# Performance work log

Hardware: AMD Instinct MI355X
Metric: run time of the kernel (lower is better)

## Reference

```python
import jax, jax.numpy as jnp
import numpy as np

D = 128            # actual_dim / embed_dim
DM = 2 * D         # d_model
HID = 2 * DM       # LSTMCell hidden size
NSYM = 200000
PAD = NSYM
B = 4096
S = 5
NB = 64
STEPS = 4
EPS = 1e-6


def setup_inputs() -> dict:
    key = jax.random.key(0)
    ks = jax.random.split(key, 24)
    def rn(k, sh, scale=0.02):
        return jax.random.normal(k, sh, dtype=jnp.float32) * scale
    emb = rn(ks[10], (NSYM + 1, D)).at[PAD].set(0.0)  # padding row zeroed
    inp = {
        'query': jax.random.randint(ks[0], (B, 2), 0, NSYM),
        'support': jax.random.randint(ks[1], (S, 2), 0, NSYM),
        'q_l_conn': jax.random.randint(ks[2], (B, NB, 2), 0, NSYM),
        'q_l_deg': jax.random.randint(ks[3], (B,), 0, NB),
        'q_r_conn': jax.random.randint(ks[4], (B, NB, 2), 0, NSYM),
        'q_r_deg': jax.random.randint(ks[5], (B,), 0, NB),
        's_l_conn': jax.random.randint(ks[6], (S, NB, 2), 0, NSYM),
        's_l_deg': jax.random.randint(ks[7], (S,), 0, NB),
        's_r_conn': jax.random.randint(ks[8], (S, NB, 2), 0, NSYM),
        's_r_deg': jax.random.randint(ks[9], (S,), 0, NB),
        'emb': emb,
        'gcn_w': rn(ks[11], (D, 2 * D)),
        'gcn_bias': jnp.zeros((D,), jnp.float32),
        'proj1_w': rn(ks[12], (2 * DM, DM)),
        'proj1_b': jnp.zeros((2 * DM,), jnp.float32),
        'proj2_w': rn(ks[13], (DM, 2 * DM)),
        'proj2_b': jnp.zeros((DM,), jnp.float32),
        'ln_g': jnp.ones((DM,), jnp.float32),
        'ln_b': jnp.zeros((DM,), jnp.float32),
        'w_ih': rn(ks[14], (4 * HID, DM)),
        'w_hh': rn(ks[15], (4 * HID, HID)),
        'b_ih': jnp.zeros((4 * HID,), jnp.float32),
        'b_hh': jnp.zeros((4 * HID,), jnp.float32),
    }
    return inp


def _neighbor_encoder(conn, deg, emb, gcn_w, gcn_bias):
    # conn: [N, NB, 2] ids (rel, ent); deg: [N]
    rel = emb[conn[:, :, 0]]                     # [N, NB, D] gather
    ent = emb[conn[:, :, 1]]                     # [N, NB, D] gather
    x = jnp.concatenate([rel, ent], axis=-1)     # [N, NB, 2D]
    out = jnp.einsum('bnd,kd->bnk', x, gcn_w) + gcn_bias  # [N, NB, D]
    denom = jnp.maximum(deg, 1).astype(out.dtype)[:, None]
    return jnp.tanh(out.sum(axis=1) / denom)     # [N, D]


def _support_encoder(x, proj1_w, proj1_b, proj2_w, proj2_b, ln_g, ln_b):
    residual = x
    h = jax.nn.relu(x @ proj1_w.T + proj1_b)
    h = h @ proj2_w.T + proj2_b
    z = h + residual
    mu = z.mean(axis=-1, keepdims=True)
    sigma = jnp.std(z, axis=-1, keepdims=True, ddof=1)
    return ln_g * (z - mu) / (sigma + EPS) + ln_b


def _query_encoder(support_vec, query, w_ih, w_hh, b_ih, b_hh):
    # support_vec: [DM] (single support prototype); query: [B, DM]
    bsz = query.shape[0]
    h_r = jnp.zeros((bsz, HID), query.dtype)
    c = jnp.zeros((bsz, HID), query.dtype)
    xW = query @ w_ih.T + b_ih  # invariant across steps
    h = query
    for _ in range(STEPS):
        gates = xW + h_r @ w_hh.T + b_hh
        i, f, g, o = jnp.split(gates, 4, axis=-1)
        c = jax.nn.sigmoid(f) * c + jax.nn.sigmoid(i) * jnp.tanh(g)
        h_cell = jax.nn.sigmoid(o) * jnp.tanh(c)
        h = query + h_cell[:, :DM]
        # attention over a single support row: softmax of one logit == 1
        r = jnp.broadcast_to(support_vec[None, :], h.shape)
        h_r = jnp.concatenate([h, r], axis=-1)
    return h


def reference(query, support, q_l_conn, q_l_deg, q_r_conn, q_r_deg,
              s_l_conn, s_l_deg, s_r_conn, s_r_deg,
              emb, gcn_w, gcn_bias, proj1_w, proj1_b, proj2_w, proj2_b,
              ln_g, ln_b, w_ih, w_hh, b_ih, b_hh):
    ql = _neighbor_encoder(q_l_conn, q_l_deg, emb, gcn_w, gcn_bias)
    qr = _neighbor_encoder(q_r_conn, q_r_deg, emb, gcn_w, gcn_bias)
    sl = _neighbor_encoder(s_l_conn, s_l_deg, emb, gcn_w, gcn_bias)
    sr = _neighbor_encoder(s_r_conn, s_r_deg, emb, gcn_w, gcn_bias)
    query_nb = jnp.concatenate([ql, qr], axis=-1)    # [B, DM]
    support_nb = jnp.concatenate([sl, sr], axis=-1)  # [S, DM]
    se = lambda x: _support_encoder(x, proj1_w, proj1_b, proj2_w, proj2_b, ln_g, ln_b)
    support_g = se(support_nb).mean(axis=0)          # [DM]
    query_g = se(query_nb)                            # [B, DM]
    query_f = _query_encoder(support_g, query_g, w_ih, w_hh, b_ih, b_hh)
    qn = query_f / jnp.maximum(jnp.linalg.norm(query_f, axis=-1, keepdims=True), 1e-12)
    sn = support_g / jnp.maximum(jnp.linalg.norm(support_g), 1e-12)
    return qn @ sn                                    # [B] matching scores
```

## Files before the change

kernel.cpp:

```cpp
#include <hip/hip_runtime.h>

#define BQ 4096
#define NS 5

typedef __attribute__((ext_vector_type(8))) short bf16x8;
typedef __attribute__((ext_vector_type(4))) float f32x4;
typedef unsigned short ushortT;

#define WS_QNB    0
#define WS_Z      1048576
#define WS_QG     2097152
#define WS_XW     3145728
#define WS_CBUF   5242880
#define WS_XS     6291456
#define WS_H1B    7348224
#define WS_ABF    7872512
#define WS_HB1    8134656
#define WS_P1B    8396800
#define WS_P2B    8462336
#define WS_WIHB   8527872
#define WS_WHHB   8658944
#define WS_GWB    8790016
#define WS_SNB    8806400
#define WS_H1G    8807680
#define WS_ZB     8810240
#define WS_SG     8811520
#define WS_SN     8811776
#define WS_SWL    8812032
#define WS_BL     8813056

__device__ __forceinline__ float wave_allreduce(float v) {
#pragma unroll
  for (int off = 32; off > 0; off >>= 1) v += __shfl_xor(v, off, 64);
  return v;
}
__device__ __forceinline__ float block_allreduce(float v, float* buf) {
  v = wave_allreduce(v);
  __syncthreads();
  if ((threadIdx.x & 63) == 0) buf[threadIdx.x >> 6] = v;
  __syncthreads();
  return buf[0] + buf[1] + buf[2] + buf[3];
}
__device__ __forceinline__ float sigm(float x) { return 1.0f / (1.0f + expf(-x)); }
__device__ __forceinline__ ushortT f2bf(float f) {
  unsigned int u = __float_as_uint(f);
  unsigned int r = (u + 0x7fffu + ((u >> 16) & 1u)) >> 16;
  return (ushortT)r;
}
__device__ __forceinline__ float bf2f(ushortT u) {
  return __uint_as_float(((unsigned int)u) << 16);
}
__device__ __forceinline__ float dot4(float4 a, float4 b) {
  return a.x * b.x + a.y * b.y + a.z * b.z + a.w * b.w;
}

__global__ __launch_bounds__(256) void k_gather(
    const int* __restrict__ qlc, const int* __restrict__ qrc,
    const int* __restrict__ slc, const int* __restrict__ src_,
    const float* __restrict__ emb, ushortT* __restrict__ XS,
    const float* __restrict__ w_ih, const float* __restrict__ w_hh,
    const float* __restrict__ p1w, const float* __restrict__ p2w,
    const float* __restrict__ gcn_w,
    const float* __restrict__ b_ih, const float* __restrict__ b_hh,
    ushortT* __restrict__ p1b16, ushortT* __restrict__ p2b16,
    ushortT* __restrict__ wihb, ushortT* __restrict__ whhb,
    ushortT* __restrict__ gwb, float* __restrict__ bL) {
  const int r = blockIdx.x;
  const int t = threadIdx.x;
  if (r >= 2 * (BQ + NS)) {
    const int gid = (r - 2 * (BQ + NS)) * 256 + t;
    const int stride = 512 * 256;
    for (int i = gid; i < 131072; i += stride) p1b16[i] = f2bf(p1w[i]);
    for (int i = gid; i < 131072; i += stride) p2b16[i] = f2bf(p2w[i]);
    for (int i = gid; i < 262144; i += stride) {
      int n = i >> 8, k = i & 255;
      int j = (n >> 2) + 512 * (n & 3);
      wihb[i] = f2bf(w_ih[j * 256 + k]);
      whhb[i] = f2bf(w_hh[j * 512 + k]);
    }
    for (int i = gid; i < 32768; i += stride) gwb[i] = f2bf(gcn_w[i]);
    for (int i = gid; i < 1024; i += stride) {
      int j = (i >> 2) + 512 * (i & 3);
      bL[i] = b_ih[j] + b_hh[j];
    }
    return;
  }
  const int b = r >> 1, side = r & 1;
  const int* cg;
  if (b < BQ) cg = (side ? qrc : qlc) + (size_t)b * 128;
  else        cg = (side ? src_ : slc) + (size_t)(b - BQ) * 128;
  __shared__ int connS[128];
  __shared__ __align__(16) float part[8][132];
  if (t < 128) connS[t] = cg[t];
  __syncthreads();
  const int s = t >> 5, l = t & 31;
  const float4* emb4 = (const float4*)emb;
  float4 acc = make_float4(0.f, 0.f, 0.f, 0.f);
#pragma unroll
  for (int kb = 0; kb < 2; kb++) {
    int im[8];
#pragma unroll
    for (int k = 0; k < 8; k++) im[k] = connS[(kb * 8 + k) * 8 + s];
    float4 v[8];
#pragma unroll
    for (int k = 0; k < 8; k++) v[k] = emb4[(size_t)im[k] * 32 + l];
#pragma unroll
    for (int k = 0; k < 8; k++) {
      acc.x += v[k].x; acc.y += v[k].y; acc.z += v[k].z; acc.w += v[k].w;
    }
  }
  *(float4*)&part[s][l * 4] = acc;
  __syncthreads();
  const int hf = t >> 7, dd = t & 127;
  float sum = part[hf][dd] + part[2 + hf][dd] + part[4 + hf][dd] + part[6 + hf][dd];
  XS[(size_t)r * 256 + t] = f2bf(sum);
}

__global__ __launch_bounds__(256) void k_gcn(
    const ushortT* __restrict__ XS, const ushortT* __restrict__ gwb,
    const float* __restrict__ gcn_bias,
    const int* __restrict__ qld, const int* __restrict__ qrd,
    const int* __restrict__ sld, const int* __restrict__ srd,
    float* __restrict__ qnb, float* __restrict__ snb, ushortT* __restrict__ xq) {
  __shared__ short As[64 * 40];
  __shared__ short Bs[128 * 40];
  __shared__ int degl[32], degr[32];
  const int t = threadIdx.x;
  const int row0 = blockIdx.x * 64;
  if (t < 32) {
    int b = (row0 >> 1) + t;
    int dl = 1, dr = 1;
    if (b < BQ) { dl = qld[b]; dr = qrd[b]; }
    else if (b < BQ + NS) { dl = sld[b - BQ]; dr = srd[b - BQ]; }
    degl[t] = (dl > 0) ? dl : 1;
    degr[t] = (dr > 0) ? dr : 1;
  }
  const int wave = t >> 6, lane = t & 63;
  const int wm = wave >> 1, wn = wave & 1, quad = lane >> 4, mr = lane & 15;
  f32x4 acc[2][4];
#pragma unroll
  for (int mi = 0; mi < 2; mi++)
#pragma unroll
    for (int ni = 0; ni < 4; ni++) acc[mi][ni] = (f32x4){0.f, 0.f, 0.f, 0.f};
  const int arow = t >> 2, akc = t & 3;
  for (int k0 = 0; k0 < 256; k0 += 32) {
    float4 av = *(const float4*)(XS + (size_t)(row0 + arow) * 256 + k0 + akc * 8);
    float4 bv0 = *(const float4*)(gwb + (size_t)arow * 256 + k0 + akc * 8);
    float4 bv1 = *(const float4*)(gwb + (size_t)(64 + arow) * 256 + k0 + akc * 8);
    __syncthreads();
    *(float4*)&As[arow * 40 + akc * 8] = av;
    *(float4*)&Bs[arow * 40 + akc * 8] = bv0;
    *(float4*)&Bs[(64 + arow) * 40 + akc * 8] = bv1;
    __syncthreads();
    bf16x8 af[2], bfr[4];
#pragma unroll
    for (int mi = 0; mi < 2; mi++)
      af[mi] = *(const bf16x8*)&As[(wm * 32 + mi * 16 + mr) * 40 + quad * 8];
#pragma unroll
    for (int ni = 0; ni < 4; ni++)
      bfr[ni] = *(const bf16x8*)&Bs[(wn * 64 + ni * 16 + mr) * 40 + quad * 8];
#pragma unroll
    for (int mi = 0; mi < 2; mi++)
#pragma unroll
      for (int ni = 0; ni < 4; ni++)
        acc[mi][ni] = __builtin_amdgcn_mfma_f32_16x16x32_bf16(af[mi], bfr[ni], acc[mi][ni], 0, 0, 0);
  }
#pragma unroll
  for (int mi = 0; mi < 2; mi++) {
#pragma unroll
    for (int ni = 0; ni < 4; ni++) {
      const int col = wn * 64 + ni * 16 + mr;
      const int rb = row0 + wm * 32 + mi * 16 + quad * 4;
      const float bs = 64.0f * gcn_bias[col];
#pragma unroll
      for (int reg = 0; reg < 4; reg++) {
        const int row = rb + reg;
        const int b = row >> 1, side = row & 1;
        if (b >= BQ + NS) continue;
        const int li = (row >> 1) - (row0 >> 1);
        const int deg = side ? degr[li] : degl[li];
        float val = tanhf((acc[mi][ni][reg] + bs) / (float)deg);
        if (b < BQ) {
          const size_t o = (size_t)b * 256 + side * 128 + col;
          qnb[o] = val;
          xq[o] = f2bf(val);
        } else {
          snb[(size_t)(b - BQ) * 256 + side * 128 + col] = val;
        }
      }
    }
  }
}

__global__ __launch_bounds__(256) void k_proj1(
    const ushortT* __restrict__ A, const ushortT* __restrict__ B,
    const float* __restrict__ bias, ushortT* __restrict__ outb,
    const float* __restrict__ snb, const float* __restrict__ p1w,
    const float* __restrict__ p1b, float* __restrict__ h1g) {
  __shared__ short As[64 * 40];
  __shared__ short Bs[128 * 40];
  const int t = threadIdx.x;
  if (blockIdx.x >= 256) {
    const int w = (blockIdx.x - 256) * 4 + (t >> 6);
    const int lane = t & 63;
    const int r = w >> 9, j = w & 511;
    float4 x = *(const float4*)&snb[r * 256 + lane * 4];
    float4 wv = *(const float4*)&p1w[(size_t)j * 256 + lane * 4];
    float s = wave_allreduce(dot4(x, wv));
    if (lane == 0) h1g[r * 512 + j] = fmaxf(s + p1b[j], 0.f);
    return;
  }
  const int bn = blockIdx.x % 4, bm = blockIdx.x / 4;
  const int row0 = bm * 64, col0 = bn * 128;
  const int wave = t >> 6, lane = t & 63;
  const int wm = wave >> 1, wn = wave & 1, quad = lane >> 4, mr = lane & 15;
  f32x4 acc[2][4];
#pragma unroll
  for (int mi = 0; mi < 2; mi++)
#pragma unroll
    for (int ni = 0; ni < 4; ni++) acc[mi][ni] = (f32x4){0.f, 0.f, 0.f, 0.f};
  const int arow = t >> 2, akc = t & 3;
  for (int k0 = 0; k0 < 256; k0 += 32) {
    float4 av = *(const float4*)(A + (size_t)(row0 + arow) * 256 + k0 + akc * 8);
    float4 bv0 = *(const float4*)(B + (size_t)(col0 + arow) * 256 + k0 + akc * 8);
    float4 bv1 = *(const float4*)(B + (size_t)(col0 + 64 + arow) * 256 + k0 + akc * 8);
    __syncthreads();
    *(float4*)&As[arow * 40 + akc * 8] = av;
    *(float4*)&Bs[arow * 40 + akc * 8] = bv0;
    *(float4*)&Bs[(64 + arow) * 40 + akc * 8] = bv1;
    __syncthreads();
    bf16x8 af[2], bfr[4];
#pragma unroll
    for (int mi = 0; mi < 2; mi++)
      af[mi] = *(const bf16x8*)&As[(wm * 32 + mi * 16 + mr) * 40 + quad * 8];
#pragma unroll
    for (int ni = 0; ni < 4; ni++)
      bfr[ni] = *(const bf16x8*)&Bs[(wn * 64 + ni * 16 + mr) * 40 + quad * 8];
#pragma unroll
    for (int mi = 0; mi < 2; mi++)
#pragma unroll
      for (int ni = 0; ni < 4; ni++)
        acc[mi][ni] = __builtin_amdgcn_mfma_f32_16x16x32_bf16(af[mi], bfr[ni], acc[mi][ni], 0, 0, 0);
  }
#pragma unroll
  for (int mi = 0; mi < 2; mi++) {
#pragma unroll
    for (int ni = 0; ni < 4; ni++) {
      const int col = col0 + wn * 64 + ni * 16 + mr;
      const int rb = row0 + wm * 32 + mi * 16 + quad * 4;
      const float bs = bias[col];
#pragma unroll
      for (int reg = 0; reg < 4; reg++) {
        const int row = rb + reg;
        outb[(size_t)row * 512 + col] = f2bf(fmaxf(acc[mi][ni][reg] + bs, 0.f));
      }
    }
  }
}

__global__ __launch_bounds__(256) void k_proj2(
    const ushortT* __restrict__ A, const ushortT* __restrict__ B,
    const float* __restrict__ bias, const float* __restrict__ aux,
    float* __restrict__ outf,
    const float* __restrict__ snb, const float* __restrict__ h1g,
    const float* __restrict__ p2w, const float* __restrict__ p2b,
    float* __restrict__ zb) {
  __shared__ short As[64 * 40];
  __shared__ short Bs[128 * 40];
  const int t = threadIdx.x;
  if (blockIdx.x >= 128) {
    const int w = (blockIdx.x - 128) * 4 + (t >> 6);
    const int lane = t & 63;
    const int r = w >> 8, tt = w & 255;
    float4 h0 = *(const float4*)&h1g[r * 512 + lane * 4];
    float4 h1 = *(const float4*)&h1g[r * 512 + 256 + lane * 4];
    float4 w0 = *(const float4*)&p2w[(size_t)tt * 512 + lane * 4];
    float4 w1 = *(const float4*)&p2w[(size_t)tt * 512 + 256 + lane * 4];
    float s = wave_allreduce(dot4(h0, w0) + dot4(h1, w1));
    if (lane == 0) zb[r * 256 + tt] = s + p2b[tt] + snb[r * 256 + tt];
    return;
  }
  const int bn = blockIdx.x % 2, bm = blockIdx.x / 2;
  const int row0 = bm * 64, col0 = bn * 128;
  const int wave = t >> 6, lane = t & 63;
  const int wm = wave >> 1, wn = wave & 1, quad = lane >> 4, mr = lane & 15;
  f32x4 acc[2][4];
#pragma unroll
  for (int mi = 0; mi < 2; mi++)
#pragma unroll
    for (int ni = 0; ni < 4; ni++) acc[mi][ni] = (f32x4){0.f, 0.f, 0.f, 0.f};
  const int arow = t >> 2, akc = t & 3;
  for (int k0 = 0; k0 < 512; k0 += 32) {
    float4 av = *(const float4*)(A + (size_t)(row0 + arow) * 512 + k0 + akc * 8);
    float4 bv0 = *(const float4*)(B + (size_t)(col0 + arow) * 512 + k0 + akc * 8);
    float4 bv1 = *(const float4*)(B + (size_t)(col0 + 64 + arow) * 512 + k0 + akc * 8);
    __syncthreads();
    *(float4*)&As[arow * 40 + akc * 8] = av;
    *(float4*)&Bs[arow * 40 + akc * 8] = bv0;
    *(float4*)&Bs[(64 + arow) * 40 + akc * 8] = bv1;
    __syncthreads();
    bf16x8 af[2], bfr[4];
#pragma unroll
    for (int mi = 0; mi < 2; mi++)
      af[mi] = *(const bf16x8*)&As[(wm * 32 + mi * 16 + mr) * 40 + quad * 8];
#pragma unroll
    for (int ni = 0; ni < 4; ni++)
      bfr[ni] = *(const bf16x8*)&Bs[(wn * 64 + ni * 16 + mr) * 40 + quad * 8];
#pragma unroll
    for (int mi = 0; mi < 2; mi++)
#pragma unroll
      for (int ni = 0; ni < 4; ni++)
        acc[mi][ni] = __builtin_amdgcn_mfma_f32_16x16x32_bf16(af[mi], bfr[ni], acc[mi][ni], 0, 0, 0);
  }
#pragma unroll
  for (int mi = 0; mi < 2; mi++) {
#pragma unroll
    for (int ni = 0; ni < 4; ni++) {
      const int col = col0 + wn * 64 + ni * 16 + mr;
      const int rb = row0 + wm * 32 + mi * 16 + quad * 4;
      const float bs = bias[col];
#pragma unroll
      for (int reg = 0; reg < 4; reg++) {
        const int row = rb + reg;
        const size_t off = (size_t)row * 256 + col;
        outf[off] = acc[mi][ni][reg] + bs + aux[off];
      }
    }
  }
}

__global__ __launch_bounds__(256) void k_ln2(
    const float* __restrict__ Z, const float* __restrict__ ln_g,
    const float* __restrict__ ln_b, float* __restrict__ qg, ushortT* __restrict__ qgb,
    const float* __restrict__ zb, float* __restrict__ sg, float* __restrict__ sn_out) {
  const int t = threadIdx.x;
  if (blockIdx.x >= BQ / 4) {
    __shared__ float rbuf[4];
    float acc = 0.f;
    for (int r = 0; r < NS; r++) {
      float z = zb[r * 256 + t];
      float s = block_allreduce(z, rbuf);
      float mu = s * (1.f / 256.f);
      float dz = z - mu;
      float s2 = block_allreduce(dz * dz, rbuf);
      float rstd = 1.f / (sqrtf(s2 * (1.f / 255.f)) + 1e-6f);
      acc += ln_g[t] * dz * rstd + ln_b[t];
      __syncthreads();
    }
    float g = acc * (1.f / (float)NS);
    sg[t] = g;
    float n2 = block_allreduce(g * g, rbuf);
    sn_out[t] = g / fmaxf(sqrtf(n2), 1e-12f);
    return;
  }
  const int row = blockIdx.x * 4 + (t >> 6);
  const int lane = t & 63;
  float4 z = *(const float4*)&Z[(size_t)row * 256 + lane * 4];
  float s = wave_allreduce(z.x + z.y + z.z + z.w);
  float mu = s * (1.f / 256.f);
  float dx = z.x - mu, dy = z.y - mu, dz = z.z - mu, dw = z.w - mu;
  float s2 = wave_allreduce(dx * dx + dy * dy + dz * dz + dw * dw);
  float rstd = 1.f / (sqrtf(s2 * (1.f / 255.f)) + 1e-6f);
  float4 g = *(const float4*)&ln_g[lane * 4];
  float4 bb = *(const float4*)&ln_b[lane * 4];
  float4 o;
  o.x = g.x * dx * rstd + bb.x;
  o.y = g.y * dy * rstd + bb.y;
  o.z = g.z * dz * rstd + bb.z;
  o.w = g.w * dw * rstd + bb.w;
  *(float4*)&qg[(size_t)row * 256 + lane * 4] = o;
  ushort4 u;
  u.x = f2bf(o.x); u.y = f2bf(o.y); u.z = f2bf(o.z); u.w = f2bf(o.w);
  *(ushort4*)&qgb[(size_t)row * 256 + lane * 4] = u;
}

__global__ __launch_bounds__(256) void k_gemm_lstm(
    const ushortT* __restrict__ A, const ushortT* __restrict__ B,
    const float* __restrict__ bL, float* __restrict__ sWl,
    const float* __restrict__ qg, ushortT* __restrict__ xwb,
    float* __restrict__ cbuf, ushortT* __restrict__ hb_out,
    const float* __restrict__ sg, const float* __restrict__ w_hh, int phase) {
  __shared__ short As[64 * 40];
  __shared__ short Bs[128 * 40];
  __shared__ __align__(16) float Cs[64 * 132];
  const int t = threadIdx.x;
  if (blockIdx.x >= 512) {
    const int n = (blockIdx.x - 512) * 4 + (t >> 6);
    const int lane = t & 63;
    const int j = (n >> 2) + 512 * (n & 3);
    float4 x = *(const float4*)&sg[lane * 4];
    float4 wv = *(const float4*)&w_hh[(size_t)j * 512 + 256 + lane * 4];
    float s = wave_allreduce(dot4(x, wv));
    if (lane == 0) sWl[n] = s;
    return;
  }
  const int bn = blockIdx.x & 7, bm = blockIdx.x >> 3;
  const int row0 = bm * 64, col0 = bn * 128;
  const int wave = t >> 6, lane = t & 63;
  const int wm = wave >> 1, wn = wave & 1, quad = lane >> 4, mr = lane & 15;
  f32x4 acc[2][4];
#pragma unroll
  for (int mi = 0; mi < 2; mi++)
#pragma unroll
    for (int ni = 0; ni < 4; ni++) acc[mi][ni] = (f32x4){0.f, 0.f, 0.f, 0.f};
  const int arow = t >> 2, akc = t & 3;
  for (int k0 = 0; k0 < 256; k0 += 32) {
    float4 av = *(const float4*)(A + (size_t)(row0 + arow) * 256 + k0 + akc * 8);
    float4 bv0 = *(const float4*)(B + (size_t)(col0 + arow) * 256 + k0 + akc * 8);
    float4 bv1 = *(const float4*)(B + (size_t)(col0 + 64 + arow) * 256 + k0 + akc * 8);
    __syncthreads();
    *(float4*)&As[arow * 40 + akc * 8] = av;
    *(float4*)&Bs[arow * 40 + akc * 8] = bv0;
    *(float4*)&Bs[(64 + arow) * 40 + akc * 8] = bv1;
    __syncthreads();
    bf16x8 af[2], bfr[4];
#pragma unroll
    for (int mi = 0; mi < 2; mi++)
      af[mi] = *(const bf16x8*)&As[(wm * 32 + mi * 16 + mr) * 40 + quad * 8];
#pragma unroll
    for (int ni = 0; ni < 4; ni++)
      bfr[ni] = *(const bf16x8*)&Bs[(wn * 64 + ni * 16 + mr) * 40 + quad * 8];
#pragma unroll
    for (int mi = 0; mi < 2; mi++)
#pragma unroll
      for (int ni = 0; ni < 4; ni++)
        acc[mi][ni] = __builtin_amdgcn_mfma_f32_16x16x32_bf16(af[mi], bfr[ni], acc[mi][ni], 0, 0, 0);
  }
#pragma unroll
  for (int mi = 0; mi < 2; mi++)
#pragma unroll
    for (int ni = 0; ni < 4; ni++)
#pragma unroll
      for (int reg = 0; reg < 4; reg++)
        Cs[(wm * 32 + mi * 16 + quad * 4 + reg) * 132 + wn * 64 + ni * 16 + mr] =
            acc[mi][ni][reg];
  __syncthreads();
  const int u = t & 31, grp = t >> 5;
  const int ugl = bn * 32 + u;
#pragma unroll
  for (int i = 0; i < 8; i++) {
    const int rl = grp * 8 + i;
    const int row = row0 + rl;
    const size_t o = (size_t)row * 256 + ugl;
    float4 gv = *(const float4*)&Cs[rl * 132 + u * 4];
    if (phase == 0) {
      float4 bb = *(const float4*)&bL[col0 + u * 4];
      gv.x += bb.x; gv.y += bb.y; gv.z += bb.z; gv.w += bb.w;
      float c0 = sigm(gv.x) * tanhf(gv.z);
      float h = qg[o] + sigm(gv.w) * tanhf(c0);
      cbuf[o] = c0;
      hb_out[o] = f2bf(h);
      ushort4 xo;
      xo.x = f2bf(gv.x); xo.y = f2bf(gv.y);
      xo.z = f2bf(gv.z); xo.w = f2bf(gv.w);
      *(ushort4*)&xwb[(size_t)row * 1024 + col0 + u * 4] = xo;
    } else {
      ushort4 xv = *(const ushort4*)&xwb[(size_t)row * 1024 + col0 + u * 4];
      float4 sv = *(const float4*)&sWl[col0 + u * 4];
      gv.x += bf2f(xv.x) + sv.x; gv.y += bf2f(xv.y) + sv.y;
      gv.z += bf2f(xv.z) + sv.z; gv.w += bf2f(xv.w) + sv.w;
      float c = sigm(gv.y) * cbuf[o] + sigm(gv.x) * tanhf(gv.z);
      float h = qg[o] + sigm(gv.w) * tanhf(c);
      if (phase == 2) {
        cbuf[o] = h;
      } else {
        cbuf[o] = c;
        hb_out[o] = f2bf(h);
      }
    }
  }
}

__global__ __launch_bounds__(256) void k_out(
    const float* __restrict__ hf, const float* __restrict__ sn, float* __restrict__ out) {
  const int t = threadIdx.x;
  const int row = blockIdx.x * 4 + (t >> 6);
  const int lane = t & 63;
  float4 h = *(const float4*)&hf[(size_t)row * 256 + lane * 4];
  float4 s = *(const float4*)&sn[lane * 4];
  float dt = wave_allreduce(dot4(h, s));
  float nr = wave_allreduce(dot4(h, h));
  if (lane == 0) out[row] = dt / fmaxf(sqrtf(nr), 1e-12f);
}

extern "C" void kernel_launch(void* const* d_in, const int* in_sizes, int n_in,
                              void* d_out, int out_size, void* d_ws, size_t ws_size,
                              hipStream_t stream) {
  const int* q_l_conn = (const int*)d_in[2];
  const int* q_l_deg  = (const int*)d_in[3];
  const int* q_r_conn = (const int*)d_in[4];
  const int* q_r_deg  = (const int*)d_in[5];
  const int* s_l_conn = (const int*)d_in[6];
  const int* s_l_deg  = (const int*)d_in[7];
  const int* s_r_conn = (const int*)d_in[8];
  const int* s_r_deg  = (const int*)d_in[9];
  const float* emb      = (const float*)d_in[10];
  const float* gcn_w    = (const float*)d_in[11];
  const float* gcn_bias = (const float*)d_in[12];
  const float* proj1_w  = (const float*)d_in[13];
  const float* proj1_b  = (const float*)d_in[14];
  const float* proj2_w  = (const float*)d_in[15];
  const float* proj2_b  = (const float*)d_in[16];
  const float* ln_g     = (const float*)d_in[17];
  const float* ln_b     = (const float*)d_in[18];
  const float* w_ih     = (const float*)d_in[19];
  const float* w_hh     = (const float*)d_in[20];
  const float* b_ih     = (const float*)d_in[21];
  const float* b_hh     = (const float*)d_in[22];

  float* ws = (float*)d_ws;
  float* qnb   = ws + WS_QNB;
  float* Z     = ws + WS_Z;
  float* qg    = ws + WS_QG;
  ushortT* xwb = (ushortT*)(ws + WS_XW);
  float* cbuf  = ws + WS_CBUF;
  ushortT* XS    = (ushortT*)(ws + WS_XS);
  ushortT* h1b   = (ushortT*)(ws + WS_H1B);
  ushortT* abf   = (ushortT*)(ws + WS_ABF);
  ushortT* hb1   = (ushortT*)(ws + WS_HB1);
  ushortT* p1b16 = (ushortT*)(ws + WS_P1B);
  ushortT* p2b16 = (ushortT*)(ws + WS_P2B);
  ushortT* wihb  = (ushortT*)(ws + WS_WIHB);
  ushortT* whhb  = (ushortT*)(ws + WS_WHHB);
  ushortT* gwb   = (ushortT*)(ws + WS_GWB);
  float* snb   = ws + WS_SNB;
  float* h1g   = ws + WS_H1G;
  float* zb    = ws + WS_ZB;
  float* sg    = ws + WS_SG;
  float* sn    = ws + WS_SN;
  float* sWl   = ws + WS_SWL;
  float* bL    = ws + WS_BL;
  float* out   = (float*)d_out;

  hipLaunchKernelGGL(k_gather, dim3(2 * (BQ + NS) + 512), dim3(256), 0, stream,
                     q_l_conn, q_r_conn, s_l_conn, s_r_conn, emb, XS,
                     w_ih, w_hh, proj1_w, proj2_w, gcn_w, b_ih, b_hh,
                     p1b16, p2b16, wihb, whhb, gwb, bL);
  hipLaunchKernelGGL(k_gcn, dim3(129), dim3(256), 0, stream,
                     XS, gwb, gcn_bias, q_l_deg, q_r_deg, s_l_deg, s_r_deg,
                     qnb, snb, abf);
  hipLaunchKernelGGL(k_proj1, dim3(256 + 640), dim3(256), 0, stream,
                     abf, p1b16, proj1_b, h1b,
                     snb, proj1_w, proj1_b, h1g);
  hipLaunchKernelGGL(k_proj2, dim3(128 + 320), dim3(256), 0, stream,
                     h1b, p2b16, proj2_b, qnb, Z,
                     snb, h1g, proj2_w, proj2_b, zb);
  hipLaunchKernelGGL(k_ln2, dim3(BQ / 4 + 1), dim3(256), 0, stream,
                     Z, ln_g, ln_b, qg, abf, zb, sg, sn);
  hipLaunchKernelGGL(k_gemm_lstm, dim3(512 + 256), dim3(256), 0, stream,
                     abf, wihb, bL, sWl, qg, xwb, cbuf, hb1, sg, w_hh, 0);
  hipLaunchKernelGGL(k_gemm_lstm, dim3(512), dim3(256), 0, stream,
                     hb1, whhb, bL, sWl, qg, xwb, cbuf, abf, sg, w_hh, 1);
  hipLaunchKernelGGL(k_gemm_lstm, dim3(512), dim3(256), 0, stream,
                     abf, whhb, bL, sWl, qg, xwb, cbuf, hb1, sg, w_hh, 1);
  hipLaunchKernelGGL(k_gemm_lstm, dim3(512), dim3(256), 0, stream,
                     hb1, whhb, bL, sWl, qg, xwb, cbuf, (ushortT*)nullptr, sg, w_hh, 2);
  hipLaunchKernelGGL(k_out, dim3(BQ / 4), dim3(256), 0, stream, cbuf, sn, out);
}
```

Before: 335.8 us.

## Convert embedding table to bf16 up front and gather half-width rows

Adds a prep pass that converts the whole fp32 embedding table to bf16 into workspace on every call, then gathers 8-byte bf16 chunks per neighbor instead of 16-byte fp32 chunks. The weight conversions move into the same prep kernel, which no longer overlaps with the gather. The goal is to halve the bytes moved by the random-row gather. The cost is a full-table read and write on each call, plus bf16 rounding of the embeddings before they are summed. A runtime workspace-size check falls back to the old fp32 gather when the buffer is too small.

```diff
diff --git a/kernel.cpp b/kernel.cpp
--- a/kernel.cpp
+++ b/kernel.cpp
@@ -28,6 +28,8 @@
 #define WS_SN     8811776
 #define WS_SWL    8812032
 #define WS_BL     8813056
+#define WS_EMB16  8814080
+#define EMB_ELEMS 25600128
 
 __device__ __forceinline__ float wave_allreduce(float v) {
 #pragma unroll
@@ -54,10 +56,8 @@
   return a.x * b.x + a.y * b.y + a.z * b.z + a.w * b.w;
 }
 
-__global__ __launch_bounds__(256) void k_gather(
-    const int* __restrict__ qlc, const int* __restrict__ qrc,
-    const int* __restrict__ slc, const int* __restrict__ src_,
-    const float* __restrict__ emb, ushortT* __restrict__ XS,
+__global__ __launch_bounds__(256) void k_prep(
+    const float* __restrict__ emb, ushortT* __restrict__ emb16, int doEmb,
     const float* __restrict__ w_ih, const float* __restrict__ w_hh,
     const float* __restrict__ p1w, const float* __restrict__ p2w,
     const float* __restrict__ gcn_w,
@@ -65,27 +65,75 @@
     ushortT* __restrict__ p1b16, ushortT* __restrict__ p2b16,
     ushortT* __restrict__ wihb, ushortT* __restrict__ whhb,
     ushortT* __restrict__ gwb, float* __restrict__ bL) {
+  const int gid = blockIdx.x * 256 + threadIdx.x;
+  const int stride = gridDim.x * 256;
+  if (doEmb) {
+    const float4* e4 = (const float4*)emb;
+    ushort4* o4 = (ushort4*)emb16;
+    for (int i = gid; i < EMB_ELEMS / 4; i += stride) {
+      float4 v = e4[i];
+      ushort4 u;
+      u.x = f2bf(v.x); u.y = f2bf(v.y); u.z = f2bf(v.z); u.w = f2bf(v.w);
+      o4[i] = u;
+    }
+  }
+  for (int i = gid; i < 131072; i += stride) p1b16[i] = f2bf(p1w[i]);
+  for (int i = gid; i < 131072; i += stride) p2b16[i] = f2bf(p2w[i]);
+  for (int i = gid; i < 262144; i += stride) {
+    int n = i >> 8, k = i & 255;
+    int j = (n >> 2) + 512 * (n & 3);
+    wihb[i] = f2bf(w_ih[j * 256 + k]);
+    whhb[i] = f2bf(w_hh[j * 512 + k]);
+  }
+  for (int i = gid; i < 32768; i += stride) gwb[i] = f2bf(gcn_w[i]);
+  for (int i = gid; i < 1024; i += stride) {
+    int j = (i >> 2) + 512 * (i & 3);
+    bL[i] = b_ih[j] + b_hh[j];
+  }
+}
+
+__global__ __launch_bounds__(256) void k_gather16(
+    const int* __restrict__ qlc, const int* __restrict__ qrc,
+    const int* __restrict__ slc, const int* __restrict__ src_,
+    const ushortT* __restrict__ emb16, ushortT* __restrict__ XS) {
   const int r = blockIdx.x;
-  const int t = threadIdx.x;
-  if (r >= 2 * (BQ + NS)) {
-    const int gid = (r - 2 * (BQ + NS)) * 256 + t;
-    const int stride = 512 * 256;
-    for (int i = gid; i < 131072; i += stride) p1b16[i] = f2bf(p1w[i]);
-    for (int i = gid; i < 131072; i += stride) p2b16[i] = f2bf(p2w[i]);
-    for (int i = gid; i < 262144; i += stride) {
-      int n = i >> 8, k = i & 255;
-      int j = (n >> 2) + 512 * (n & 3);
-      wihb[i] = f2bf(w_ih[j * 256 + k]);
-      whhb[i] = f2bf(w_hh[j * 512 + k]);
-    }
-    for (int i = gid; i < 32768; i += stride) gwb[i] = f2bf(gcn_w[i]);
-    for (int i = gid; i < 1024; i += stride) {
-      int j = (i >> 2) + 512 * (i & 3);
-      bL[i] = b_ih[j] + b_hh[j];
-    }
-    return;
-  }
   const int b = r >> 1, side = r & 1;
+  const int t = threadIdx.x;
+  const int* cg;
+  if (b < BQ) cg = (side ? qrc : qlc) + (size_t)b * 128;
+  else        cg = (side ? src_ : slc) + (size_t)(b - BQ) * 128;
+  __shared__ int connS[128];
+  __shared__ __align__(16) float part[8][132];
+  if (t < 128) connS[t] = cg[t];
+  __syncthreads();
+  const int s = t >> 5, l = t & 31;
+  const ushort4* e2 = (const ushort4*)emb16;
+  float4 acc = make_float4(0.f, 0.f, 0.f, 0.f);
+  int im[16];
+#pragma unroll
+  for (int k = 0; k < 16; k++) im[k] = connS[k * 8 + s];
+  ushort4 v[16];
+#pragma unroll
+  for (int k = 0; k < 16; k++) v[k] = e2[(size_t)im[k] * 32 + l];
+#pragma unroll
+  for (int k = 0; k < 16; k++) {
+    acc.x += bf2f(v[k].x); acc.y += bf2f(v[k].y);
+    acc.z += bf2f(v[k].z); acc.w += bf2f(v[k].w);
+  }
+  *(float4*)&part[s][l * 4] = acc;
+  __syncthreads();
+  const int hf = t >> 7, dd = t & 127;
+  float sum = part[hf][dd] + part[2 + hf][dd] + part[4 + hf][dd] + part[6 + hf][dd];
+  XS[(size_t)r * 256 + t] = f2bf(sum);
+}
+
+__global__ __launch_bounds__(256) void k_gather32(
+    const int* __restrict__ qlc, const int* __restrict__ qrc,
+    const int* __restrict__ slc, const int* __restrict__ src_,
+    const float* __restrict__ emb, ushortT* __restrict__ XS) {
+  const int r = blockIdx.x;
+  const int b = r >> 1, side = r & 1;
+  const int t = threadIdx.x;
   const int* cg;
   if (b < BQ) cg = (side ? qrc : qlc) + (size_t)b * 128;
   else        cg = (side ? src_ : slc) + (size_t)(b - BQ) * 128;
@@ -530,12 +578,23 @@
   float* sn    = ws + WS_SN;
   float* sWl   = ws + WS_SWL;
   float* bL    = ws + WS_BL;
+  ushortT* emb16 = (ushortT*)(ws + WS_EMB16);
   float* out   = (float*)d_out;
 
-  hipLaunchKernelGGL(k_gather, dim3(2 * (BQ + NS) + 512), dim3(256), 0, stream,
-                     q_l_conn, q_r_conn, s_l_conn, s_r_conn, emb, XS,
+  const size_t needF = (size_t)WS_EMB16 + (EMB_ELEMS + 1) / 2;
+  const int useBf16 = (ws_size >= needF * sizeof(float)) ? 1 : 0;
+
+  hipLaunchKernelGGL(k_prep, dim3(2048), dim3(256), 0, stream,
+                     emb, emb16, useBf16,
                      w_ih, w_hh, proj1_w, proj2_w, gcn_w, b_ih, b_hh,
                      p1b16, p2b16, wihb, whhb, gwb, bL);
+  if (useBf16) {
+    hipLaunchKernelGGL(k_gather16, dim3(2 * (BQ + NS)), dim3(256), 0, stream,
+                       q_l_conn, q_r_conn, s_l_conn, s_r_conn, emb16, XS);
+  } else {
+    hipLaunchKernelGGL(k_gather32, dim3(2 * (BQ + NS)), dim3(256), 0, stream,
+                       q_l_conn, q_r_conn, s_l_conn, s_r_conn, emb, XS);
+  }
   hipLaunchKernelGGL(k_gcn, dim3(129), dim3(256), 0, stream,
                      XS, gwb, gcn_bias, q_l_deg, q_r_deg, s_l_deg, s_r_deg,
                      qnb, snb, abf);
```

Result: no change. 333.1 us (-0.8%).
